# Optimization experiments

Measured on AMD Instinct MI355X. Metric: run time of the kernel, lower is better.

The kernel has to match this reference:

```python
import jax, jax.numpy as jnp
import numpy as np

B, C, P, L = 128, 5, 5, 5
D = 128
USER_NUM, TITLE_NUM, ENTITY_NUM, REL_NUM = 50000, 30000, 100000, 100


def setup_inputs() -> dict:
    key = jax.random.key(0)
    k = jax.random.split(key, 22)
    f = jnp.float32
    s = 0.1  # weight scale to keep LSTM gates in a sane range
    return {
        "candidate_newsindex": jax.random.randint(k[0], (B, C), 0, TITLE_NUM),
        "user_index": jax.random.randint(k[1], (B,), 0, USER_NUM),
        "total_paths_index": jax.random.randint(k[2], (USER_NUM, C, P, L), 0, TITLE_NUM),
        "total_type_index": jax.random.randint(k[3], (USER_NUM, C, P, L), 0, 3),
        "total_relations_index": jax.random.randint(k[4], (USER_NUM, C, P, L), 0, REL_NUM),
        "entity_emb": jax.random.normal(k[5], (ENTITY_NUM, D), f),
        "relation_emb": jax.random.normal(k[6], (REL_NUM, D), f),
        "user_emb": jax.random.normal(k[7], (USER_NUM, D), f),
        "news_emb": jax.random.normal(k[8], (TITLE_NUM, D), f),
        "type_emb": jax.random.normal(k[9], (3, D), f),
        "Wih0": jax.random.normal(k[10], (P, 4 * D, 3 * D), f) * s,
        "Whh0": jax.random.normal(k[11], (P, 4 * D, D), f) * s,
        "bih0": jax.random.normal(k[12], (P, 4 * D), f) * s,
        "bhh0": jax.random.normal(k[13], (P, 4 * D), f) * s,
        "Wih1": jax.random.normal(k[14], (P, 4 * D, D), f) * s,
        "Whh1": jax.random.normal(k[15], (P, 4 * D, D), f) * s,
        "bih1": jax.random.normal(k[16], (P, 4 * D), f) * s,
        "bhh1": jax.random.normal(k[17], (P, 4 * D), f) * s,
        "W1": jax.random.normal(k[18], (16, D), f) * s,
        "b1": jax.random.normal(k[19], (16,), f) * s,
        "W2": jax.random.normal(k[20], (1, 16), f) * s,
        "b2": jax.random.normal(k[21], (1,), f) * s,
    }


def _lstm2(x, Wih0, Whh0, bih0, bhh0, Wih1, Whh1, bih1, bhh1):
    """2-layer PyTorch-style LSTM (gate order i,f,g,o). x: [N, T, in] -> [N, T, H]."""
    def layer(x, Wih, Whh, bih, bhh):
        N = x.shape[0]
        H = Whh.shape[1]
        h0 = jnp.zeros((N, H), x.dtype)
        c0 = jnp.zeros((N, H), x.dtype)
        b = bih + bhh
        def step(carry, xt):
            h, c = carry
            g = xt @ Wih.T + h @ Whh.T + b
            i, f, gg, o = jnp.split(g, 4, axis=-1)
            c = jax.nn.sigmoid(f) * c + jax.nn.sigmoid(i) * jnp.tanh(gg)
            h = jax.nn.sigmoid(o) * jnp.tanh(c)
            return (h, c), h
        _, ys = jax.lax.scan(step, (h0, c0), x.swapaxes(0, 1))
        return ys.swapaxes(0, 1)
    x = layer(x, Wih0, Whh0, bih0, bhh0)
    x = layer(x, Wih1, Whh1, bih1, bhh1)
    return x


def reference(candidate_newsindex, user_index, total_paths_index, total_type_index,
              total_relations_index, entity_emb, relation_emb, user_emb, news_emb,
              type_emb, Wih0, Whh0, bih0, bhh0, Wih1, Whh1, bih1, bhh1,
              W1, b1, W2, b2):
    bpath = total_paths_index[user_index]  # [B,C,P,L]
    btype = total_type_index[user_index]
    brel = total_relations_index[user_index]
    # per-node embedding selected by type: 0->user, 1->news, else entity
    node = jnp.where((btype == 0)[..., None], user_emb[bpath],
                     jnp.where((btype == 1)[..., None], news_emb[bpath], entity_emb[bpath]))
    inp = jnp.concatenate([node, type_emb[btype], relation_emb[brel]], axis=-1)  # [B,C,P,L,3D]
    Bb, Cc, Pp, Ll, F = inp.shape
    x = inp.transpose(2, 0, 1, 3, 4).reshape(Pp, Bb * Cc, Ll, F)  # per-path batches
    outs = jax.vmap(_lstm2)(x, Wih0, Whh0, bih0, bhh0, Wih1, Whh1, bih1, bhh1)  # [P,BC,L,H]
    idx = jnp.arange(Pp)
    sel = outs[idx, :, idx, :]  # LSTM i's output at timestep i -> [P, BC, H]
    ps = jax.nn.sigmoid(jnp.maximum(sel @ W1.T + b1, 0.0) @ W2.T + b2)[..., 0]  # [P,BC]
    ps_mean = ps.reshape(Pp, Bb, Cc).mean(axis=0)  # [B,C]
    # faithful to source: total_output accumulates over candidates j, so the score
    # for candidate j is the cumulative mean of path scores for candidates 0..j
    total_score = jnp.cumsum(ps_mean, axis=1) / jnp.arange(1, Cc + 1, dtype=ps_mean.dtype)
    emb_score = jax.nn.sigmoid(jnp.sum(news_emb[candidate_newsindex] * user_emb[user_index][:, None, :], axis=-1))
    return emb_score + total_score
```

## Files before the change

### kernel.cpp

```cpp
#include <hip/hip_runtime.h>
#include <math.h>

#define BB   128
#define CC   5
#define PP   5
#define LL   5
#define DD   128
#define NSEQ 640
#define GATES 512
#define IN0  384
#define HPAD 136

typedef __attribute__((ext_vector_type(8))) short short8;
typedef __attribute__((ext_vector_type(4))) float f32x4;

__device__ __forceinline__ float sigf(float x){ return 1.0f/(1.0f+__expf(-x)); }
__device__ __forceinline__ float tanhfast(float x){ return 1.0f - 2.0f/(__expf(2.0f*x)+1.0f); }

__device__ __forceinline__ unsigned short f2bf(float x){
    union { float f; unsigned u; } v; v.f = x;
    unsigned r = v.u + 0x7FFF + ((v.u >> 16) & 1);
    return (unsigned short)(r >> 16);
}

__device__ __constant__ int c_ptmap[15] = {0,5,6,10,11,12,15,16,17,18,20,21,22,23,24};

__global__ void stage0_kernel(const float* __restrict__ Wih0, const float* __restrict__ Whh0,
                              const float* __restrict__ Wih1, const float* __restrict__ Whh1,
                              const float* __restrict__ bih0, const float* __restrict__ bhh0,
                              const float* __restrict__ bih1, const float* __restrict__ bhh1,
                              unsigned short* __restrict__ F0, unsigned short* __restrict__ F1,
                              unsigned short* __restrict__ F2, unsigned short* __restrict__ F3,
                              float* __restrict__ b0, float* __restrict__ b1c,
                              float* __restrict__ psum,
                              const int* __restrict__ user_index,
                              const int* __restrict__ tpath, const int* __restrict__ ttype,
                              const int* __restrict__ trel,
                              const float* __restrict__ entity_emb, const float* __restrict__ relation_emb,
                              const float* __restrict__ user_emb, const float* __restrict__ news_emb,
                              const float* __restrict__ type_emb,
                              unsigned short* __restrict__ X){
    int bx = blockIdx.x;
    if (bx < 985){
        int id = bx*256 + threadIdx.x;
        const int NF0 = PP*12*32*64;
        const int NFH = PP*4*32*64;
        if (id < NF0 + 3*NFH){
            const float* src; unsigned short* dst; int K, KT, fid;
            if (id < NF0){ src = Wih0; dst = F0; K = IN0; KT = 12; fid = id; }
            else {
                int j = id - NF0; int m = j / NFH; fid = j % NFH; K = DD; KT = 4;
                src = (m==0)?Whh0:(m==1)?Wih1:Whh1;
                dst = (m==0)?F1:(m==1)?F2:F3;
            }
            int lane = fid & 63; int rem = fid >> 6;
            int gt = rem & 31; rem >>= 5;
            int kt = rem % KT; int p = rem / KT;
            int g  = gt*16 + (lane & 15);
            int k0 = kt*32 + (lane >> 4)*8;
            const float* s = src + (size_t)(p*GATES + g)*K + k0;
            float4 x0 = *(const float4*)s;
            float4 x1 = *(const float4*)(s+4);
            uint4 o;
            o.x = f2bf(x0.x) | ((unsigned)f2bf(x0.y)<<16);
            o.y = f2bf(x0.z) | ((unsigned)f2bf(x0.w)<<16);
            o.z = f2bf(x1.x) | ((unsigned)f2bf(x1.y)<<16);
            o.w = f2bf(x1.z) | ((unsigned)f2bf(x1.w)<<16);
            *(uint4*)(dst + (size_t)fid*8) = o;
        } else {
            int j = id - (NF0 + 3*NFH);
            if (j < PP*GATES) b0[j] = bih0[j] + bhh0[j];
            else if (j < 2*PP*GATES){ int q = j - PP*GATES; b1c[q] = bih1[q] + bhh1[q]; }
            else if (j < 2*PP*GATES + NSEQ){ psum[j - 2*PP*GATES] = 0.0f; }
        }
    } else {
        int id = (bx - 985)*256 + threadIdx.x;
        if (id >= 15*NSEQ*48) return;
        int ptIdx = id / (NSEQ*48); int rem = id % (NSEQ*48);
        int n = rem / 48, q = rem % 48;
        int pt = c_ptmap[ptIdx];
        int p = pt / LL, t = pt % LL;
        int b = n / CC, c = n % CC;
        int u = user_index[b];
        int base = ((u*CC + c)*PP + p)*LL + t;
        int col = q*8;
        const float* s;
        if (q < 16){
            int ty = ttype[base]; int pi = tpath[base];
            const float* e = (ty==0)?user_emb:(ty==1)?news_emb:entity_emb;
            s = e + (size_t)pi*DD + col;
        } else if (q < 32){
            s = type_emb + (size_t)ttype[base]*DD + (col-128);
        } else {
            s = relation_emb + (size_t)trel[base]*DD + (col-256);
        }
        float4 x0 = *(const float4*)s, x1 = *(const float4*)(s+4);
        uint4 o;
        o.x = f2bf(x0.x) | ((unsigned)f2bf(x0.y)<<16);
        o.y = f2bf(x0.z) | ((unsigned)f2bf(x0.w)<<16);
        o.z = f2bf(x1.x) | ((unsigned)f2bf(x1.y)<<16);
        o.w = f2bf(x1.z) | ((unsigned)f2bf(x1.w)<<16);
        *(uint4*)(X + (size_t)(pt*NSEQ + n)*IN0 + col) = o;
    }
}

__global__ __launch_bounds__(256) void gemm_ih0_v5(const unsigned short* __restrict__ X,
                                                   const unsigned short* __restrict__ F0,
                                                   float* __restrict__ G0c){
    __shared__ unsigned short Bs[12*4*512];
    int bx = blockIdx.x;
    int nch = bx & 7;
    int m64 = (bx >> 3) % 10;
    int pt  = c_ptmap[bx / 80];
    int p = pt / LL;
    int tid = threadIdx.x, lane = tid & 63, w = tid >> 6;
    int r16 = lane & 15, qd = lane >> 4;

    const unsigned short* Fp = F0 + (((size_t)p*12)*32 + nch*4)*512;
    uint4 breg[12];
    #pragma unroll
    for (int j=0;j<12;j++)
        breg[j] = *(const uint4*)(Fp + (size_t)j*32*512 + tid*8);
    #pragma unroll
    for (int j=0;j<12;j++)
        *(uint4*)(Bs + j*2048 + tid*8) = breg[j];
    __syncthreads();

    f32x4 acc[4];
    #pragma unroll
    for (int i=0;i<4;i++) acc[i] = (f32x4)0.0f;
    const unsigned short* Xb = X + ((size_t)pt*NSEQ + m64*64 + w*16 + r16)*IN0 + qd*8;
    #pragma unroll
    for (int kt=0; kt<12; kt++){
        short8 a = *(const short8*)(Xb + kt*32);
        #pragma unroll
        for (int i=0;i<4;i++){
            short8 bfr = *(const short8*)(Bs + (kt*4+i)*512 + lane*8);
            acc[i] = __builtin_amdgcn_mfma_f32_16x16x32_bf16(a, bfr, acc[i], 0,0,0);
        }
    }
    int tile16 = pt*40 + m64*4 + w;
    float* dst = G0c + (((size_t)tile16*32 + nch*4)*64 + lane)*4;
    #pragma unroll
    for (int i=0;i<4;i++)
        *(f32x4*)(dst + (size_t)i*256) = acc[i];
}

__global__ __launch_bounds__(512, 2) void lstm_v7(
    const float* __restrict__ G0c,
    const unsigned short* __restrict__ F1,
    const unsigned short* __restrict__ F2,
    const unsigned short* __restrict__ F3,
    const float* __restrict__ b0, const float* __restrict__ b1c,
    const float* __restrict__ W1, const float* __restrict__ b1v,
    const float* __restrict__ W2, const float* __restrict__ b2v,
    float* __restrict__ psum){
    __shared__ unsigned short h0T[2][16*HPAD];
    __shared__ unsigned short h1T[2][16*HPAD];
    __shared__ float h1f[16*132];
    __shared__ float mlpb[16*17];

    int p = blockIdx.x / 40, nt = blockIdx.x % 40;
    int n0 = nt*16;
    int tid = threadIdx.x;
    int lane = tid & 63, w = tid >> 6;
    int r16 = lane & 15, qd = lane >> 4;
    int j = w*16 + r16;

    short8 f1r[16], f2r[16], f3r[16];
    {
        const unsigned short* F1p = F1 + (size_t)p*4*32*512 + lane*8;
        const unsigned short* F2p = F2 + (size_t)p*4*32*512 + lane*8;
        const unsigned short* F3p = F3 + (size_t)p*4*32*512 + lane*8;
        #pragma unroll
        for (int kt=0; kt<4; kt++)
            #pragma unroll
            for (int i=0;i<4;i++){
                f1r[kt*4+i] = *(const short8*)(F1p + (size_t)(kt*32 + i*8 + w)*512);
                f2r[kt*4+i] = *(const short8*)(F2p + (size_t)(kt*32 + i*8 + w)*512);
                f3r[kt*4+i] = *(const short8*)(F3p + (size_t)(kt*32 + i*8 + w)*512);
            }
    }
    float bL0[4], bL1[4];
    #pragma unroll
    for (int i=0;i<4;i++){
        int col = (i*8 + w)*16 + r16;
        bL0[i] = b0[p*GATES + col];
        bL1[i] = b1c[p*GATES + col];
    }

    f32x4 pf[4];
    {
        const float* slab = G0c + (size_t)((p*LL + 0)*40 + nt)*8192;
        #pragma unroll
        for (int i=0;i<4;i++) pf[i] = *(const f32x4*)(slab + ((i*8+w)*64 + lane)*4);
    }
    float c0s[4] = {0,0,0,0}, c1s[4] = {0,0,0,0};

    for (int t=0; t<=p; t++){
        int cur = t & 1, prv = cur ^ 1;
        f32x4 acc[4];
        #pragma unroll
        for (int i=0;i<4;i++){
            f32x4 a = pf[i]; float bb = bL0[i];
            a[0]+=bb; a[1]+=bb; a[2]+=bb; a[3]+=bb; acc[i]=a;
        }
        if (t < p){
            const float* ns = G0c + (size_t)((p*LL + t + 1)*40 + nt)*8192;
            #pragma unroll
            for (int i=0;i<4;i++) pf[i] = *(const f32x4*)(ns + ((i*8+w)*64 + lane)*4);
        }
        if (t > 0){
            #pragma unroll
            for (int kt=0; kt<4; kt++){
                short8 a = *(const short8*)(h0T[prv] + r16*HPAD + kt*32 + qd*8);
                #pragma unroll
                for (int i=0;i<4;i++)
                    acc[i] = __builtin_amdgcn_mfma_f32_16x16x32_bf16(a, f1r[kt*4+i], acc[i], 0,0,0);
            }
        }
        #pragma unroll
        for (int v=0; v<4; v++){
            float cc = sigf(acc[1][v])*c0s[v] + sigf(acc[0][v])*tanhfast(acc[2][v]);
            c0s[v] = cc;
            h0T[cur][(qd*4+v)*HPAD + j] = f2bf(sigf(acc[3][v])*tanhfast(cc));
        }
        __syncthreads();
        #pragma unroll
        for (int i=0;i<4;i++){
            float bb = bL1[i];
            f32x4 a; a[0]=bb; a[1]=bb; a[2]=bb; a[3]=bb; acc[i]=a;
        }
        #pragma unroll
        for (int kt=0; kt<4; kt++){
            short8 a = *(const short8*)(h0T[cur] + r16*HPAD + kt*32 + qd*8);
            #pragma unroll
            for (int i=0;i<4;i++)
                acc[i] = __builtin_amdgcn_mfma_f32_16x16x32_bf16(a, f2r[kt*4+i], acc[i], 0,0,0);
        }
        if (t > 0){
            #pragma unroll
            for (int kt=0; kt<4; kt++){
                short8 a = *(const short8*)(h1T[prv] + r16*HPAD + kt*32 + qd*8);
                #pragma unroll
                for (int i=0;i<4;i++)
                    acc[i] = __builtin_amdgcn_mfma_f32_16x16x32_bf16(a, f3r[kt*4+i], acc[i], 0,0,0);
            }
        }
        #pragma unroll
        for (int v=0; v<4; v++){
            float cc = sigf(acc[1][v])*c1s[v] + sigf(acc[0][v])*tanhfast(acc[2][v]);
            c1s[v] = cc;
            float hh = sigf(acc[3][v])*tanhfast(cc);
            if (t < p) h1T[cur][(qd*4+v)*HPAD + j] = f2bf(hh);
            else       h1f[(qd*4+v)*132 + j] = hh;
        }
        __syncthreads();
    }
    if (tid < 256){
        int rr = tid & 15, hc = tid >> 4;
        const float* w1r = W1 + hc*DD;
        float acc = b1v[hc];
        #pragma unroll 4
        for (int k=0;k<DD;k++) acc = fmaf(h1f[rr*132 + k], w1r[k], acc);
        mlpb[hc*17 + rr] = fmaxf(acc, 0.0f);
    }
    __syncthreads();
    if (tid < 16){
        float s = b2v[0];
        #pragma unroll
        for (int h=0;h<16;h++) s = fmaf(mlpb[h*17 + tid], W2[h], s);
        atomicAdd(&psum[n0 + tid], 0.2f*sigf(s));
    }
}

__global__ void final_kernel(const int* __restrict__ cand, const int* __restrict__ user_index,
                             const float* __restrict__ news_emb, const float* __restrict__ user_emb,
                             const float* __restrict__ psum, float* __restrict__ out){
    int b = blockIdx.x;
    int lane = threadIdx.x;
    int u = user_index[b];
    const float* ue = user_emb + (size_t)u*DD;
    float cum = 0.0f;
    for (int c=0;c<CC;c++){
        int nb = cand[b*CC + c];
        const float* ne = news_emb + (size_t)nb*DD;
        float v = ne[lane]*ue[lane] + ne[lane+64]*ue[lane+64];
        #pragma unroll
        for (int off=32; off; off>>=1) v += __shfl_down(v, off, 64);
        if (lane == 0){
            cum += psum[b*CC + c];
            out[b*CC + c] = sigf(v) + cum/(float)(c+1);
        }
    }
}

extern "C" void kernel_launch(void* const* d_in, const int* in_sizes, int n_in,
                              void* d_out, int out_size, void* d_ws, size_t ws_size,
                              hipStream_t stream){
    const int* cand        = (const int*)d_in[0];
    const int* uidx        = (const int*)d_in[1];
    const int* tpath       = (const int*)d_in[2];
    const int* ttype       = (const int*)d_in[3];
    const int* trel        = (const int*)d_in[4];
    const float* entity_emb   = (const float*)d_in[5];
    const float* relation_emb = (const float*)d_in[6];
    const float* user_emb     = (const float*)d_in[7];
    const float* news_emb     = (const float*)d_in[8];
    const float* type_emb     = (const float*)d_in[9];
    const float* Wih0 = (const float*)d_in[10];
    const float* Whh0 = (const float*)d_in[11];
    const float* bih0 = (const float*)d_in[12];
    const float* bhh0 = (const float*)d_in[13];
    const float* Wih1 = (const float*)d_in[14];
    const float* Whh1 = (const float*)d_in[15];
    const float* bih1 = (const float*)d_in[16];
    const float* bhh1 = (const float*)d_in[17];
    const float* W1 = (const float*)d_in[18];
    const float* b1 = (const float*)d_in[19];
    const float* W2 = (const float*)d_in[20];
    const float* b2 = (const float*)d_in[21];
    float* out = (float*)d_out;

    char* ws = (char*)d_ws;
    unsigned short* F0 = (unsigned short*)ws;  ws += (size_t)PP*12*32*512*2;
    unsigned short* F1 = (unsigned short*)ws;  ws += (size_t)PP*4*32*512*2;
    unsigned short* F2 = (unsigned short*)ws;  ws += (size_t)PP*4*32*512*2;
    unsigned short* F3 = (unsigned short*)ws;  ws += (size_t)PP*4*32*512*2;
    float* b0  = (float*)ws;                   ws += PP*GATES*4;
    float* b1c = (float*)ws;                   ws += PP*GATES*4;
    unsigned short* X = (unsigned short*)ws;   ws += (size_t)PP*LL*NSEQ*IN0*2;
    float* G0c = (float*)ws;                   ws += (size_t)PP*LL*NSEQ*GATES*4;
    float* psum = (float*)ws;                  ws += NSEQ*4;

    stage0_kernel<<<985+1800,256,0,stream>>>(Wih0,Whh0,Wih1,Whh1,bih0,bhh0,bih1,bhh1,
                                             F0,F1,F2,F3,b0,b1c,psum,
                                             uidx,tpath,ttype,trel,entity_emb,relation_emb,
                                             user_emb,news_emb,type_emb,X);
    gemm_ih0_v5<<<1200,256,0,stream>>>(X, F0, G0c);
    lstm_v7<<<200,512,0,stream>>>(G0c, F1, F2, F3, b0, b1c, W1, b1, W2, b2, psum);
    final_kernel<<<BB,64,0,stream>>>(cand, uidx, news_emb, user_emb, psum, out);
}
```

Baseline: 235.9 us.

## Fuse input-projection GEMM into LSTM kernel with 64-row tiles

Removes the separate layer-0 input GEMM kernel and its fp32 G0c intermediate buffer. Each LSTM block now handles 64 sequences instead of 16 and computes X·Wih0 inline every timestep, streaming the F0/F1/F3 weights from global memory rather than keeping F1/F3 in registers. This drops a kernel launch and a large global write and read. In exchange the grid shrinks from 200 to 50 blocks, leaving most CUs idle, and the input-projection GEMM now sits on the serial per-timestep critical path, with a risk of register pressure from the 4x4 accumulator tiles.

```diff
diff --git a/kernel.cpp b/kernel.cpp
--- a/kernel.cpp
+++ b/kernel.cpp
@@ -21,6 +21,9 @@
     union { float f; unsigned u; } v; v.f = x;
     unsigned r = v.u + 0x7FFF + ((v.u >> 16) & 1);
     return (unsigned short)(r >> 16);
+}
+__device__ __forceinline__ float bf2f(unsigned short u){
+    union { unsigned u; float f; } v; v.u = ((unsigned)u) << 16; return v.f;
 }
 
 __device__ __constant__ int c_ptmap[15] = {0,5,6,10,11,12,15,16,17,18,20,21,22,23,24};
@@ -104,50 +107,9 @@
     }
 }
 
-__global__ __launch_bounds__(256) void gemm_ih0_v5(const unsigned short* __restrict__ X,
-                                                   const unsigned short* __restrict__ F0,
-                                                   float* __restrict__ G0c){
-    __shared__ unsigned short Bs[12*4*512];
-    int bx = blockIdx.x;
-    int nch = bx & 7;
-    int m64 = (bx >> 3) % 10;
-    int pt  = c_ptmap[bx / 80];
-    int p = pt / LL;
-    int tid = threadIdx.x, lane = tid & 63, w = tid >> 6;
-    int r16 = lane & 15, qd = lane >> 4;
-
-    const unsigned short* Fp = F0 + (((size_t)p*12)*32 + nch*4)*512;
-    uint4 breg[12];
-    #pragma unroll
-    for (int j=0;j<12;j++)
-        breg[j] = *(const uint4*)(Fp + (size_t)j*32*512 + tid*8);
-    #pragma unroll
-    for (int j=0;j<12;j++)
-        *(uint4*)(Bs + j*2048 + tid*8) = breg[j];
-    __syncthreads();
-
-    f32x4 acc[4];
-    #pragma unroll
-    for (int i=0;i<4;i++) acc[i] = (f32x4)0.0f;
-    const unsigned short* Xb = X + ((size_t)pt*NSEQ + m64*64 + w*16 + r16)*IN0 + qd*8;
-    #pragma unroll
-    for (int kt=0; kt<12; kt++){
-        short8 a = *(const short8*)(Xb + kt*32);
-        #pragma unroll
-        for (int i=0;i<4;i++){
-            short8 bfr = *(const short8*)(Bs + (kt*4+i)*512 + lane*8);
-            acc[i] = __builtin_amdgcn_mfma_f32_16x16x32_bf16(a, bfr, acc[i], 0,0,0);
-        }
-    }
-    int tile16 = pt*40 + m64*4 + w;
-    float* dst = G0c + (((size_t)tile16*32 + nch*4)*64 + lane)*4;
-    #pragma unroll
-    for (int i=0;i<4;i++)
-        *(f32x4*)(dst + (size_t)i*256) = acc[i];
-}
-
-__global__ __launch_bounds__(512, 2) void lstm_v7(
-    const float* __restrict__ G0c,
+__global__ __launch_bounds__(512, 2) void mega_lstm(
+    const unsigned short* __restrict__ X,
+    const unsigned short* __restrict__ F0,
     const unsigned short* __restrict__ F1,
     const unsigned short* __restrict__ F2,
     const unsigned short* __restrict__ F3,
@@ -155,31 +117,25 @@
     const float* __restrict__ W1, const float* __restrict__ b1v,
     const float* __restrict__ W2, const float* __restrict__ b2v,
     float* __restrict__ psum){
-    __shared__ unsigned short h0T[2][16*HPAD];
-    __shared__ unsigned short h1T[2][16*HPAD];
-    __shared__ float h1f[16*132];
-    __shared__ float mlpb[16*17];
-
-    int p = blockIdx.x / 40, nt = blockIdx.x % 40;
-    int n0 = nt*16;
+    __shared__ unsigned short h0T[64*HPAD];
+    __shared__ unsigned short h1T[64*HPAD];
+    __shared__ float mlpb[64*17];
+
+    int p = blockIdx.x / 10, n64 = blockIdx.x % 10;
+    int n0 = n64*64;
     int tid = threadIdx.x;
     int lane = tid & 63, w = tid >> 6;
     int r16 = lane & 15, qd = lane >> 4;
     int j = w*16 + r16;
 
-    short8 f1r[16], f2r[16], f3r[16];
+    short8 f2r[16];
     {
-        const unsigned short* F1p = F1 + (size_t)p*4*32*512 + lane*8;
         const unsigned short* F2p = F2 + (size_t)p*4*32*512 + lane*8;
-        const unsigned short* F3p = F3 + (size_t)p*4*32*512 + lane*8;
         #pragma unroll
         for (int kt=0; kt<4; kt++)
             #pragma unroll
-            for (int i=0;i<4;i++){
-                f1r[kt*4+i] = *(const short8*)(F1p + (size_t)(kt*32 + i*8 + w)*512);
+            for (int i=0;i<4;i++)
                 f2r[kt*4+i] = *(const short8*)(F2p + (size_t)(kt*32 + i*8 + w)*512);
-                f3r[kt*4+i] = *(const short8*)(F3p + (size_t)(kt*32 + i*8 + w)*512);
-            }
     }
     float bL0[4], bL1[4];
     #pragma unroll
@@ -188,88 +144,124 @@
         bL0[i] = b0[p*GATES + col];
         bL1[i] = b1c[p*GATES + col];
     }
-
-    f32x4 pf[4];
+    const unsigned short* F0p = F0 + (size_t)p*12*32*512 + lane*8;
+    const unsigned short* F1p = F1 + (size_t)p*4*32*512 + lane*8;
+    const unsigned short* F3p = F3 + (size_t)p*4*32*512 + lane*8;
+
+    float c0s[4][4] = {{0}}, c1s[4][4] = {{0}};
+
+    for (int t=0; t<=p; t++){
+        f32x4 acc[4][4];
+        #pragma unroll
+        for (int m=0;m<4;m++)
+            #pragma unroll
+            for (int i=0;i<4;i++){
+                float bb = bL0[i];
+                f32x4 a; a[0]=bb; a[1]=bb; a[2]=bb; a[3]=bb; acc[m][i]=a;
+            }
+        const unsigned short* Xb = X + ((size_t)((p*LL+t)*NSEQ) + n0)*IN0 + qd*8;
+        #pragma unroll
+        for (int kt=0; kt<12; kt++){
+            short8 bfr[4];
+            #pragma unroll
+            for (int i=0;i<4;i++)
+                bfr[i] = *(const short8*)(F0p + (size_t)(kt*32 + i*8 + w)*512);
+            #pragma unroll
+            for (int m=0;m<4;m++){
+                short8 a = *(const short8*)(Xb + (size_t)(m*16 + r16)*IN0 + kt*32);
+                #pragma unroll
+                for (int i=0;i<4;i++)
+                    acc[m][i] = __builtin_amdgcn_mfma_f32_16x16x32_bf16(a, bfr[i], acc[m][i], 0,0,0);
+            }
+        }
+        if (t > 0){
+            #pragma unroll
+            for (int kt=0; kt<4; kt++){
+                short8 bfr[4];
+                #pragma unroll
+                for (int i=0;i<4;i++)
+                    bfr[i] = *(const short8*)(F1p + (size_t)(kt*32 + i*8 + w)*512);
+                #pragma unroll
+                for (int m=0;m<4;m++){
+                    short8 a = *(const short8*)(h0T + (size_t)(m*16 + r16)*HPAD + kt*32 + qd*8);
+                    #pragma unroll
+                    for (int i=0;i<4;i++)
+                        acc[m][i] = __builtin_amdgcn_mfma_f32_16x16x32_bf16(a, bfr[i], acc[m][i], 0,0,0);
+                }
+            }
+        }
+        __syncthreads();
+        #pragma unroll
+        for (int m=0;m<4;m++)
+            #pragma unroll
+            for (int v=0; v<4; v++){
+                float cc = sigf(acc[m][1][v])*c0s[m][v] + sigf(acc[m][0][v])*tanhfast(acc[m][2][v]);
+                c0s[m][v] = cc;
+                h0T[(m*16 + qd*4 + v)*HPAD + j] = f2bf(sigf(acc[m][3][v])*tanhfast(cc));
+            }
+        __syncthreads();
+        #pragma unroll
+        for (int m=0;m<4;m++)
+            #pragma unroll
+            for (int i=0;i<4;i++){
+                float bb = bL1[i];
+                f32x4 a; a[0]=bb; a[1]=bb; a[2]=bb; a[3]=bb; acc[m][i]=a;
+            }
+        #pragma unroll
+        for (int kt=0; kt<4; kt++){
+            #pragma unroll
+            for (int m=0;m<4;m++){
+                short8 a = *(const short8*)(h0T + (size_t)(m*16 + r16)*HPAD + kt*32 + qd*8);
+                #pragma unroll
+                for (int i=0;i<4;i++)
+                    acc[m][i] = __builtin_amdgcn_mfma_f32_16x16x32_bf16(a, f2r[kt*4+i], acc[m][i], 0,0,0);
+            }
+        }
+        if (t > 0){
+            #pragma unroll
+            for (int kt=0; kt<4; kt++){
+                short8 bfr[4];
+                #pragma unroll
+                for (int i=0;i<4;i++)
+                    bfr[i] = *(const short8*)(F3p + (size_t)(kt*32 + i*8 + w)*512);
+                #pragma unroll
+                for (int m=0;m<4;m++){
+                    short8 a = *(const short8*)(h1T + (size_t)(m*16 + r16)*HPAD + kt*32 + qd*8);
+                    #pragma unroll
+                    for (int i=0;i<4;i++)
+                        acc[m][i] = __builtin_amdgcn_mfma_f32_16x16x32_bf16(a, bfr[i], acc[m][i], 0,0,0);
+                }
+            }
+        }
+        __syncthreads();
+        #pragma unroll
+        for (int m=0;m<4;m++)
+            #pragma unroll
+            for (int v=0; v<4; v++){
+                float cc = sigf(acc[m][1][v])*c1s[m][v] + sigf(acc[m][0][v])*tanhfast(acc[m][2][v]);
+                c1s[m][v] = cc;
+                h1T[(m*16 + qd*4 + v)*HPAD + j] = f2bf(sigf(acc[m][3][v])*tanhfast(cc));
+            }
+    }
+    __syncthreads();
     {
-        const float* slab = G0c + (size_t)((p*LL + 0)*40 + nt)*8192;
-        #pragma unroll
-        for (int i=0;i<4;i++) pf[i] = *(const f32x4*)(slab + ((i*8+w)*64 + lane)*4);
-    }
-    float c0s[4] = {0,0,0,0}, c1s[4] = {0,0,0,0};
-
-    for (int t=0; t<=p; t++){
-        int cur = t & 1, prv = cur ^ 1;
-        f32x4 acc[4];
-        #pragma unroll
-        for (int i=0;i<4;i++){
-            f32x4 a = pf[i]; float bb = bL0[i];
-            a[0]+=bb; a[1]+=bb; a[2]+=bb; a[3]+=bb; acc[i]=a;
-        }
-        if (t < p){
-            const float* ns = G0c + (size_t)((p*LL + t + 1)*40 + nt)*8192;
-            #pragma unroll
-            for (int i=0;i<4;i++) pf[i] = *(const f32x4*)(ns + ((i*8+w)*64 + lane)*4);
-        }
-        if (t > 0){
-            #pragma unroll
-            for (int kt=0; kt<4; kt++){
-                short8 a = *(const short8*)(h0T[prv] + r16*HPAD + kt*32 + qd*8);
-                #pragma unroll
-                for (int i=0;i<4;i++)
-                    acc[i] = __builtin_amdgcn_mfma_f32_16x16x32_bf16(a, f1r[kt*4+i], acc[i], 0,0,0);
-            }
-        }
-        #pragma unroll
-        for (int v=0; v<4; v++){
-            float cc = sigf(acc[1][v])*c0s[v] + sigf(acc[0][v])*tanhfast(acc[2][v]);
-            c0s[v] = cc;
-            h0T[cur][(qd*4+v)*HPAD + j] = f2bf(sigf(acc[3][v])*tanhfast(cc));
-        }
-        __syncthreads();
-        #pragma unroll
-        for (int i=0;i<4;i++){
-            float bb = bL1[i];
-            f32x4 a; a[0]=bb; a[1]=bb; a[2]=bb; a[3]=bb; acc[i]=a;
-        }
-        #pragma unroll
-        for (int kt=0; kt<4; kt++){
-            short8 a = *(const short8*)(h0T[cur] + r16*HPAD + kt*32 + qd*8);
-            #pragma unroll
-            for (int i=0;i<4;i++)
-                acc[i] = __builtin_amdgcn_mfma_f32_16x16x32_bf16(a, f2r[kt*4+i], acc[i], 0,0,0);
-        }
-        if (t > 0){
-            #pragma unroll
-            for (int kt=0; kt<4; kt++){
-                short8 a = *(const short8*)(h1T[prv] + r16*HPAD + kt*32 + qd*8);
-                #pragma unroll
-                for (int i=0;i<4;i++)
-                    acc[i] = __builtin_amdgcn_mfma_f32_16x16x32_bf16(a, f3r[kt*4+i], acc[i], 0,0,0);
-            }
-        }
-        #pragma unroll
-        for (int v=0; v<4; v++){
-            float cc = sigf(acc[1][v])*c1s[v] + sigf(acc[0][v])*tanhfast(acc[2][v]);
-            c1s[v] = cc;
-            float hh = sigf(acc[3][v])*tanhfast(cc);
-            if (t < p) h1T[cur][(qd*4+v)*HPAD + j] = f2bf(hh);
-            else       h1f[(qd*4+v)*132 + j] = hh;
-        }
-        __syncthreads();
-    }
-    if (tid < 256){
-        int rr = tid & 15, hc = tid >> 4;
-        const float* w1r = W1 + hc*DD;
-        float acc = b1v[hc];
-        #pragma unroll 4
-        for (int k=0;k<DD;k++) acc = fmaf(h1f[rr*132 + k], w1r[k], acc);
-        mlpb[hc*17 + rr] = fmaxf(acc, 0.0f);
+        int rr = tid & 63, hc0 = tid >> 6;
+        const unsigned short* hrow = h1T + rr*HPAD;
+        #pragma unroll
+        for (int s=0; s<2; s++){
+            int hc = hc0 + s*8;
+            const float* w1r = W1 + hc*DD;
+            float acc = b1v[hc];
+            #pragma unroll 4
+            for (int k=0;k<DD;k++) acc = fmaf(bf2f(hrow[k]), w1r[k], acc);
+            mlpb[rr*17 + hc] = fmaxf(acc, 0.0f);
+        }
     }
     __syncthreads();
-    if (tid < 16){
+    if (tid < 64){
         float s = b2v[0];
         #pragma unroll
-        for (int h=0;h<16;h++) s = fmaf(mlpb[h*17 + tid], W2[h], s);
+        for (int h=0;h<16;h++) s = fmaf(mlpb[tid*17 + h], W2[h], s);
         atomicAdd(&psum[n0 + tid], 0.2f*sigf(s));
     }
 }
@@ -330,14 +322,12 @@
     float* b0  = (float*)ws;                   ws += PP*GATES*4;
     float* b1c = (float*)ws;                   ws += PP*GATES*4;
     unsigned short* X = (unsigned short*)ws;   ws += (size_t)PP*LL*NSEQ*IN0*2;
-    float* G0c = (float*)ws;                   ws += (size_t)PP*LL*NSEQ*GATES*4;
     float* psum = (float*)ws;                  ws += NSEQ*4;
 
     stage0_kernel<<<985+1800,256,0,stream>>>(Wih0,Whh0,Wih1,Whh1,bih0,bhh0,bih1,bhh1,
                                              F0,F1,F2,F3,b0,b1c,psum,
                                              uidx,tpath,ttype,trel,entity_emb,relation_emb,
                                              user_emb,news_emb,type_emb,X);
-    gemm_ih0_v5<<<1200,256,0,stream>>>(X, F0, G0c);
-    lstm_v7<<<200,512,0,stream>>>(G0c, F1, F2, F3, b0, b1c, W1, b1, W2, b2, psum);
+    mega_lstm<<<50,512,0,stream>>>(X, F0, F1, F2, F3, b0, b1c, W1, b1, W2, b2, psum);
     final_kernel<<<BB,64,0,stream>>>(cand, uidx, news_emb, user_emb, psum, out);
 }
```

Measured after the change: 396.4 us. +68.1%, slower.
